# Performance work log

Hardware: AMD Instinct MI355X
Metric: run time of the kernel (lower is better)

## Reference

```python
import jax, jax.numpy as jnp
import numpy as np

B, N, M, F, D, OUT = 2, 8192, 8192, 128, 3, 512

def setup_inputs() -> dict:
    key = jax.random.key(0)
    k1, k2, k3, k4, k5 = jax.random.split(key, 5)
    return {
        'geometry': jax.random.normal(k1, (B, N, D), dtype=jnp.float32),
        'gaussian_pcd': jax.random.normal(k2, (B, M, D), dtype=jnp.float32),
        'features': jax.random.normal(k3, (B, M, F), dtype=jnp.float32),
        'W_proj': jax.random.normal(k4, (OUT, F), dtype=jnp.float32) / np.sqrt(F),
        'b_proj': jax.random.normal(k5, (OUT,), dtype=jnp.float32) * 0.01,
        'k': 10,
    }

def reference(geometry, gaussian_pcd, features, W_proj, b_proj, k):
    # cdist via ||q||^2 + ||p||^2 - 2 q.p (matches torch.cdist matmul mode)
    q2 = jnp.sum(geometry * geometry, axis=-1)            # [B,N]
    p2 = jnp.sum(gaussian_pcd * gaussian_pcd, axis=-1)    # [B,M]
    d2 = q2[:, :, None] + p2[:, None, :] - 2.0 * jnp.einsum('bnd,bmd->bnm', geometry, gaussian_pcd)
    dists = jnp.sqrt(jnp.maximum(d2, 0.0))                # [B,N,M]
    # k smallest, sorted ascending
    neg_d, idx = jax.lax.top_k(-dists, k)                 # [B,N,k]
    knn_d = -neg_d
    # gather knn features: [B,N,k,F]
    knn_f = jax.vmap(lambda f, i: f[i])(features, idx)
    # inverse-distance weights, normalized
    w = 1.0 / (knn_d + 1e-8)
    w = w / jnp.sum(w, axis=-1, keepdims=True)
    interp = jnp.einsum('bnk,bnkf->bnf', w, knn_f)        # [B,N,F]
    # gaussian_feature_proj: Linear(128 -> feature_dim)
    return jnp.einsum('bnf,of->bno', interp, W_proj) + b_proj
```

## Files before the change

### kernel.cpp

```cpp
#include <hip/hip_runtime.h>
#include <math.h>

#define NQ   8192
#define NP   8192
#define NF   128
#define NOUT 512
#define NB   2
#define KNN  10
#define BNQ  (NB*NQ)
#define QW   4

typedef unsigned long long u64;

__device__ __forceinline__ u64 shfl64(u64 v, int src) {
  unsigned lo = (unsigned)__shfl((int)(unsigned)(v & 0xffffffffull), src, 64);
  unsigned hi = (unsigned)__shfl((int)(unsigned)(v >> 32), src, 64);
  return ((u64)hi << 32) | lo;
}
__device__ __forceinline__ u64 shflup64(u64 v) {
  unsigned lo = (unsigned)__shfl_up((int)(unsigned)(v & 0xffffffffull), 1, 64);
  unsigned hi = (unsigned)__shfl_up((int)(unsigned)(v >> 32), 1, 64);
  return ((u64)hi << 32) | lo;
}

__device__ __forceinline__ float dist2m(float m2x, float m2y, float m2z,
                                        float q2c, float4 p) {
  return fmaf(m2x, p.x, fmaf(m2y, p.y, fmaf(m2z, p.z, q2c + p.w)));
}

__device__ __forceinline__ float wmin64f(float v) {
#pragma unroll
  for (int off = 1; off < 64; off <<= 1)
    v = fminf(v, __shfl_xor(v, off, 64));
  return v;
}

__global__ __launch_bounds__(256) void prep_kernel(
    const float* __restrict__ gpcd, const float* __restrict__ W,
    float4* __restrict__ pts4, float* __restrict__ Wt)
{
  int tid = blockIdx.x * 256 + threadIdx.x;
  if (tid < NB * NP) {
    const float* p = gpcd + (size_t)tid * 3;
    float x = p[0], y = p[1], z = p[2];
    float p2 = x * x + y * y + z * z;
    pts4[tid] = make_float4(x, y, z, p2);
  }
  int o = tid >> 7, f = tid & 127;
  Wt[(size_t)f * NOUT + o] = W[tid];
}

__global__ __launch_bounds__(256) void knn_interp_kernel(
    const float* __restrict__ geometry, const float4* __restrict__ pts4,
    const float* __restrict__ features, float* __restrict__ At)
{
  const int lane = threadIdx.x & 63;
  const int wave = (blockIdx.x << 2) | (threadIdx.x >> 6);
  const int q0   = wave * QW;
  const int b    = q0 >> 13;
  const float4* __restrict__ P = pts4 + ((size_t)b << 13);

  float m2x[QW], m2y[QW], m2z[QW], q2[QW];
#pragma unroll
  for (int j = 0; j < QW; ++j) {
    const float* g = geometry + (size_t)(q0 + j) * 3;
    float x = g[0], y = g[1], z = g[2];
    q2[j]  = x * x + y * y + z * z;
    m2x[j] = -2.0f * x; m2y[j] = -2.0f * y; m2z[j] = -2.0f * z;
  }

  float lmin[QW];
#pragma unroll
  for (int j = 0; j < QW; ++j) lmin[j] = INFINITY;
#pragma unroll 2
  for (int t = 0; t < NP / 64; ++t) {
    const float4 p = P[(t << 6) | lane];
#pragma unroll
    for (int j = 0; j < QW; ++j)
      lmin[j] = fminf(lmin[j], dist2m(m2x[j], m2y[j], m2z[j], q2[j], p));
  }
#pragma unroll
  for (int j = 0; j < QW; ++j) lmin[j] = fmaxf(lmin[j], 0.0f);

  float theta[QW];
#pragma unroll
  for (int j = 0; j < QW; ++j) {
    float lm  = lmin[j];
    float tau = 0.0f;
#pragma unroll
    for (int r = 0; r < KNN; ++r) {
      tau = wmin64f(lm);
      u64 mk = __ballot(lm == tau);
      int w  = __builtin_ctzll(mk);
      if (lane == w) lm = INFINITY;
    }
    theta[j] = __uint_as_float(__float_as_uint(tau) + 1);
  }

  u64   list[QW];
  float dl[QW];
#pragma unroll
  for (int j = 0; j < QW; ++j) {
    list[j] = 0x7F800000FFFFFFFFull;
    dl[j]   = INFINITY;
  }
  const float qnan = __builtin_nanf("");

  for (int t = 0; t < NP / 64; ++t) {
    const float4 p = P[(t << 6) | lane];
#pragma unroll
    for (int j = 0; j < QW; ++j) {
      float d2 = dist2m(m2x[j], m2y[j], m2z[j], q2[j], p);
      for (;;) {
        u64 mask = __ballot(d2 < theta[j]);
        if (!mask) break;
        int src = __builtin_ctzll(mask);
        float cd = __uint_as_float(
            (unsigned)__builtin_amdgcn_readlane(__float_as_int(d2), src));
        cd = fmaxf(cd, 0.0f);
        u64 kk = ((u64)__float_as_uint(cd) << 32) | (unsigned)((t << 6) + src);
        u64   prev  = shflup64(list[j]);
        float prevd = __shfl(dl[j], lane - 1, 64);
        bool mylt = list[j] < kk;
        bool pins = (lane == 0) || (prev < kk);
        list[j] = mylt ? list[j] : (pins ? kk : prev);
        dl[j]   = mylt ? dl[j]  : (pins ? cd : prevd);
        theta[j] = fminf(theta[j], __uint_as_float(
            (unsigned)__builtin_amdgcn_readlane(__float_as_int(dl[j]), 9)));
        if (lane == src) d2 = qnan;
      }
    }
  }

  const float* __restrict__ F = features + (size_t)b * NP * NF;
#pragma unroll
  for (int j = 0; j < QW; ++j) {
    float w = 1.0f / (sqrtf(dl[j]) + 1e-8f);
    float wsum = 0.0f;
#pragma unroll
    for (int jj = 0; jj < KNN; ++jj) wsum += __shfl(w, jj, 64);

    float a0 = 0.0f, a1 = 0.0f;
#pragma unroll
    for (int jj = 0; jj < KNN; ++jj) {
      float wj = __shfl(w, jj, 64) / wsum;
      int  mi  = (int)(unsigned)(shfl64(list[j], jj) & 0xffffffffull);
      const float2 f2 = *(const float2*)(F + (size_t)mi * NF + (lane << 1));
      a0 = fmaf(wj, f2.x, a0);
      a1 = fmaf(wj, f2.y, a1);
    }
    At[(size_t)(lane << 1) * BNQ + (q0 + j)]       = a0;
    At[(size_t)((lane << 1) + 1) * BNQ + (q0 + j)] = a1;
  }
}

#define PKC  64
#define PLD  68

__global__ __launch_bounds__(256) void proj_kernel(
    const float* __restrict__ At, const float* __restrict__ Wt,
    const float* __restrict__ bias, float* __restrict__ out)
{
  __shared__ __align__(16) float lds_a[PKC][PLD];
  __shared__ __align__(16) float lds_b[PKC][PLD];

  const int mt = blockIdx.x & 255;
  const int ot = blockIdx.x >> 8;
  const int tx = threadIdx.x & 15;
  const int ty = threadIdx.x >> 4;
  const int m0 = mt << 6;
  const int o0 = ot << 6;

  const int lr = threadIdx.x >> 4;
  const int lc = (threadIdx.x & 15) << 2;

  float acc[4][4];
#pragma unroll
  for (int i = 0; i < 4; ++i)
#pragma unroll
    for (int jj = 0; jj < 4; ++jj) acc[i][jj] = 0.0f;

#pragma unroll
  for (int kc = 0; kc < NF / PKC; ++kc) {
    const int k0 = kc * PKC;
#pragma unroll
    for (int rp = 0; rp < 4; ++rp) {
      const int r = (rp << 4) + lr;
      const float4 a4 = *(const float4*)(At + (size_t)(k0 + r) * BNQ  + m0 + lc);
      const float4 b4 = *(const float4*)(Wt + (size_t)(k0 + r) * NOUT + o0 + lc);
      *(float4*)(&lds_a[r][lc]) = a4;
      *(float4*)(&lds_b[r][lc]) = b4;
    }
    __syncthreads();
#pragma unroll 8
    for (int k = 0; k < PKC; ++k) {
      const float4 a  = *(const float4*)(&lds_a[k][ty << 2]);
      const float4 bv = *(const float4*)(&lds_b[k][tx << 2]);
      float av[4] = {a.x, a.y, a.z, a.w};
      float bw[4] = {bv.x, bv.y, bv.z, bv.w};
#pragma unroll
      for (int i = 0; i < 4; ++i)
#pragma unroll
        for (int jj = 0; jj < 4; ++jj)
          acc[i][jj] = fmaf(av[i], bw[jj], acc[i][jj]);
    }
    __syncthreads();
  }

  const float4 bb = *(const float4*)(bias + o0 + (tx << 2));
  float bias4[4] = {bb.x, bb.y, bb.z, bb.w};
#pragma unroll
  for (int i = 0; i < 4; ++i) {
    float4 r;
    r.x = acc[i][0] + bias4[0];
    r.y = acc[i][1] + bias4[1];
    r.z = acc[i][2] + bias4[2];
    r.w = acc[i][3] + bias4[3];
    *(float4*)(out + (size_t)(m0 + (ty << 2) + i) * NOUT + o0 + (tx << 2)) = r;
  }
}

extern "C" void kernel_launch(void* const* d_in, const int* in_sizes, int n_in,
                              void* d_out, int out_size, void* d_ws, size_t ws_size,
                              hipStream_t stream) {
  const float* geometry = (const float*)d_in[0];
  const float* gpcd     = (const float*)d_in[1];
  const float* features = (const float*)d_in[2];
  const float* W        = (const float*)d_in[3];
  const float* bias     = (const float*)d_in[4];
  float* out = (float*)d_out;

  char*   ws   = (char*)d_ws;
  float*  At   = (float*)ws;
  float4* pts4 = (float4*)(ws + (size_t)NF * BNQ * 4);
  float*  Wt   = (float*)(ws + (size_t)NF * BNQ * 4 + (size_t)NB * NP * 16);

  prep_kernel<<<256, 256, 0, stream>>>(gpcd, W, pts4, Wt);
  knn_interp_kernel<<<BNQ / (QW * 4), 256, 0, stream>>>(geometry, pts4, features, At);
  proj_kernel<<<(BNQ / 64) * (NOUT / 64), 256, 0, stream>>>(At, Wt, bias, out);
}
```

Baseline: 130.3 us.

## Split point scan across two waves per query group and merge top-k lists

Each group of four queries is now processed by two waves, each scanning half of the point cloud and building its own sorted top-k list. The two partial lists are written to shared memory and merged with a rank-based merge, then each wave performs the feature gather for two of the four queries. This doubles the number of waves to improve latency hiding and occupancy on the long distance scan. In exchange it adds block synchronization and a merge step, and the per-half threshold is looser so more insertion iterations may occur.

```diff
diff --git a/kernel.cpp b/kernel.cpp
--- a/kernel.cpp
+++ b/kernel.cpp
@@ -3,6 +3,7 @@
 
 #define NQ   8192
 #define NP   8192
+#define NPH  4096
 #define NF   128
 #define NOUT 512
 #define NB   2
@@ -12,11 +13,6 @@
 
 typedef unsigned long long u64;
 
-__device__ __forceinline__ u64 shfl64(u64 v, int src) {
-  unsigned lo = (unsigned)__shfl((int)(unsigned)(v & 0xffffffffull), src, 64);
-  unsigned hi = (unsigned)__shfl((int)(unsigned)(v >> 32), src, 64);
-  return ((u64)hi << 32) | lo;
-}
 __device__ __forceinline__ u64 shflup64(u64 v) {
   unsigned lo = (unsigned)__shfl_up((int)(unsigned)(v & 0xffffffffull), 1, 64);
   unsigned hi = (unsigned)__shfl_up((int)(unsigned)(v >> 32), 1, 64);
@@ -33,6 +29,28 @@
   for (int off = 1; off < 64; off <<= 1)
     v = fminf(v, __shfl_xor(v, off, 64));
   return v;
+}
+
+__device__ __forceinline__ void insert_loop(float d2, int idxbase, int lane,
+                                            u64& lst, float& dlv, float& th) {
+  for (;;) {
+    u64 mask = __ballot(d2 < th);
+    if (!mask) break;
+    int src = __builtin_ctzll(mask);
+    float cd = __uint_as_float(
+        (unsigned)__builtin_amdgcn_readlane(__float_as_int(d2), src));
+    cd = fmaxf(cd, 0.0f);
+    u64 kk = ((u64)__float_as_uint(cd) << 32) | (unsigned)(idxbase + src);
+    u64   prev  = shflup64(lst);
+    float prevd = __shfl(dlv, lane - 1, 64);
+    bool mylt = lst < kk;
+    bool pins = (lane == 0) || (prev < kk);
+    lst = mylt ? lst : (pins ? kk : prev);
+    dlv = mylt ? dlv : (pins ? cd : prevd);
+    th = fminf(th, __uint_as_float(
+        (unsigned)__builtin_amdgcn_readlane(__float_as_int(dlv), 9)));
+    if (lane == src) d2 = __builtin_nanf("");
+  }
 }
 
 __global__ __launch_bounds__(256) void prep_kernel(
@@ -54,17 +72,23 @@
     const float* __restrict__ geometry, const float4* __restrict__ pts4,
     const float* __restrict__ features, float* __restrict__ At)
 {
+  __shared__ u64 cand[2][QW][2][12];
+  __shared__ u64 merged[2][2][2][12];
+
   const int lane = threadIdx.x & 63;
-  const int wave = (blockIdx.x << 2) | (threadIdx.x >> 6);
-  const int q0   = wave * QW;
+  const int wid  = threadIdx.x >> 6;
+  const int g    = wid >> 1;
+  const int h    = wid & 1;
+  const int q0   = (blockIdx.x * 2 + g) * QW;
   const int b    = q0 >> 13;
-  const float4* __restrict__ P = pts4 + ((size_t)b << 13);
+  const float4* __restrict__ Ph = pts4 + ((size_t)b << 13) + (h << 12);
+  const int hbase = h << 12;
 
   float m2x[QW], m2y[QW], m2z[QW], q2[QW];
 #pragma unroll
   for (int j = 0; j < QW; ++j) {
-    const float* g = geometry + (size_t)(q0 + j) * 3;
-    float x = g[0], y = g[1], z = g[2];
+    const float* gp = geometry + (size_t)(q0 + j) * 3;
+    float x = gp[0], y = gp[1], z = gp[2];
     q2[j]  = x * x + y * y + z * z;
     m2x[j] = -2.0f * x; m2y[j] = -2.0f * y; m2z[j] = -2.0f * z;
   }
@@ -72,12 +96,14 @@
   float lmin[QW];
 #pragma unroll
   for (int j = 0; j < QW; ++j) lmin[j] = INFINITY;
-#pragma unroll 2
-  for (int t = 0; t < NP / 64; ++t) {
-    const float4 p = P[(t << 6) | lane];
+  for (int t = 0; t < NPH / 128; ++t) {
+    const float4 pa = Ph[(t << 7) | lane];
+    const float4 pb = Ph[(t << 7) | 64 | lane];
 #pragma unroll
     for (int j = 0; j < QW; ++j)
-      lmin[j] = fminf(lmin[j], dist2m(m2x[j], m2y[j], m2z[j], q2[j], p));
+      lmin[j] = fminf(lmin[j],
+                      fminf(dist2m(m2x[j], m2y[j], m2z[j], q2[j], pa),
+                            dist2m(m2x[j], m2y[j], m2z[j], q2[j], pb)));
   }
 #pragma unroll
   for (int j = 0; j < QW; ++j) lmin[j] = fmaxf(lmin[j], 0.0f);
@@ -104,53 +130,67 @@
     list[j] = 0x7F800000FFFFFFFFull;
     dl[j]   = INFINITY;
   }
-  const float qnan = __builtin_nanf("");
-
-  for (int t = 0; t < NP / 64; ++t) {
-    const float4 p = P[(t << 6) | lane];
+
+  for (int t = 0; t < NPH / 128; ++t) {
+    const float4 pa = Ph[(t << 7) | lane];
+    const float4 pb = Ph[(t << 7) | 64 | lane];
 #pragma unroll
     for (int j = 0; j < QW; ++j) {
-      float d2 = dist2m(m2x[j], m2y[j], m2z[j], q2[j], p);
-      for (;;) {
-        u64 mask = __ballot(d2 < theta[j]);
-        if (!mask) break;
-        int src = __builtin_ctzll(mask);
-        float cd = __uint_as_float(
-            (unsigned)__builtin_amdgcn_readlane(__float_as_int(d2), src));
-        cd = fmaxf(cd, 0.0f);
-        u64 kk = ((u64)__float_as_uint(cd) << 32) | (unsigned)((t << 6) + src);
-        u64   prev  = shflup64(list[j]);
-        float prevd = __shfl(dl[j], lane - 1, 64);
-        bool mylt = list[j] < kk;
-        bool pins = (lane == 0) || (prev < kk);
-        list[j] = mylt ? list[j] : (pins ? kk : prev);
-        dl[j]   = mylt ? dl[j]  : (pins ? cd : prevd);
-        theta[j] = fminf(theta[j], __uint_as_float(
-            (unsigned)__builtin_amdgcn_readlane(__float_as_int(dl[j]), 9)));
-        if (lane == src) d2 = qnan;
+      float da = dist2m(m2x[j], m2y[j], m2z[j], q2[j], pa);
+      insert_loop(da, hbase + (t << 7), lane, list[j], dl[j], theta[j]);
+      float db = dist2m(m2x[j], m2y[j], m2z[j], q2[j], pb);
+      insert_loop(db, hbase + (t << 7) + 64, lane, list[j], dl[j], theta[j]);
+    }
+  }
+
+#pragma unroll
+  for (int j = 0; j < QW; ++j)
+    if (lane < KNN) cand[g][j][h][lane] = list[j];
+  __syncthreads();
+
+#pragma unroll
+  for (int jo = 0; jo < 2; ++jo) {
+    const int jj = (h << 1) | jo;
+    const bool isA = lane < KNN;
+    const bool isB = (lane >= 16) && (lane < 16 + KNN);
+    const int  li  = isA ? lane : lane - 16;
+    if (isA | isB) {
+      u64 key = cand[g][jj][isA ? 0 : 1][li];
+      int pos = li;
+#pragma unroll
+      for (int m = 0; m < KNN; ++m) {
+        u64 other = cand[g][jj][isA ? 1 : 0][m];
+        pos += (other < key) ? 1 : 0;
       }
-    }
-  }
+      if (pos < KNN) merged[g][h][jo][pos] = key;
+    }
+  }
+  __syncthreads();
 
   const float* __restrict__ F = features + (size_t)b * NP * NF;
 #pragma unroll
-  for (int j = 0; j < QW; ++j) {
-    float w = 1.0f / (sqrtf(dl[j]) + 1e-8f);
+  for (int jo = 0; jo < 2; ++jo) {
+    u64 k = merged[g][h][jo][lane < KNN ? lane : 0];
+    float mdl = __uint_as_float((unsigned)(k >> 32));
+    int  midx = (int)(unsigned)(k & 0xffffffffull);
+
+    float w = 1.0f / (sqrtf(mdl) + 1e-8f);
     float wsum = 0.0f;
 #pragma unroll
-    for (int jj = 0; jj < KNN; ++jj) wsum += __shfl(w, jj, 64);
+    for (int jj2 = 0; jj2 < KNN; ++jj2) wsum += __shfl(w, jj2, 64);
 
     float a0 = 0.0f, a1 = 0.0f;
 #pragma unroll
-    for (int jj = 0; jj < KNN; ++jj) {
-      float wj = __shfl(w, jj, 64) / wsum;
-      int  mi  = (int)(unsigned)(shfl64(list[j], jj) & 0xffffffffull);
+    for (int jj2 = 0; jj2 < KNN; ++jj2) {
+      float wj = __shfl(w, jj2, 64) / wsum;
+      int  mi  = __shfl(midx, jj2, 64);
       const float2 f2 = *(const float2*)(F + (size_t)mi * NF + (lane << 1));
       a0 = fmaf(wj, f2.x, a0);
       a1 = fmaf(wj, f2.y, a1);
     }
-    At[(size_t)(lane << 1) * BNQ + (q0 + j)]       = a0;
-    At[(size_t)((lane << 1) + 1) * BNQ + (q0 + j)] = a1;
+    const int q = q0 + (h << 1) + jo;
+    At[(size_t)(lane << 1) * BNQ + q]       = a0;
+    At[(size_t)((lane << 1) + 1) * BNQ + q] = a1;
   }
 }
 
@@ -236,6 +276,6 @@
   float*  Wt   = (float*)(ws + (size_t)NF * BNQ * 4 + (size_t)NB * NP * 16);
 
   prep_kernel<<<256, 256, 0, stream>>>(gpcd, W, pts4, Wt);
-  knn_interp_kernel<<<BNQ / (QW * 4), 256, 0, stream>>>(geometry, pts4, features, At);
+  knn_interp_kernel<<<BNQ / 8, 256, 0, stream>>>(geometry, pts4, features, At);
   proj_kernel<<<(BNQ / 64) * (NOUT / 64), 256, 0, stream>>>(At, Wt, bias, out);
 }
```

Result: slower. 151.2 us (+16.0%).

## Drop per-query norm from distance scan and add wave-level early-skip check

Applied to the files above, without the earlier changes.

Distances are computed without the query's squared norm, which is constant per query and does not change the ordering. Signed values are handled by a monotone float-to-uint key, and the norm is added back only when the final weights are computed. The point scan now loads four points per iteration. A cheap ballot over the minimum across the four queries skips the per-query insertion loops when no lane can beat any threshold. This cuts FMAs and ballot overhead in the second pass, at the cost of more registers and more intricate handling of negative-threshold edge cases.

```diff
diff --git a/kernel.cpp b/kernel.cpp
--- a/kernel.cpp
+++ b/kernel.cpp
@@ -23,9 +23,14 @@
   return ((u64)hi << 32) | lo;
 }
 
-__device__ __forceinline__ float dist2m(float m2x, float m2y, float m2z,
-                                        float q2c, float4 p) {
-  return fmaf(m2x, p.x, fmaf(m2y, p.y, fmaf(m2z, p.z, q2c + p.w)));
+__device__ __forceinline__ float dist2s(float m2x, float m2y, float m2z,
+                                        float4 p) {
+  return fmaf(m2x, p.x, fmaf(m2y, p.y, fmaf(m2z, p.z, p.w)));
+}
+
+__device__ __forceinline__ unsigned fmono(float f) {
+  unsigned u = __float_as_uint(f);
+  return u ^ ((unsigned)((int)u >> 31) | 0x80000000u);
 }
 
 __device__ __forceinline__ float wmin64f(float v) {
@@ -33,6 +38,27 @@
   for (int off = 1; off < 64; off <<= 1)
     v = fminf(v, __shfl_xor(v, off, 64));
   return v;
+}
+
+__device__ __forceinline__ void insert_loop(float d2, int idxbase, int lane,
+                                            u64& lst, float& dlv, float& th) {
+  for (;;) {
+    u64 mask = __ballot(d2 < th);
+    if (!mask) break;
+    int src = __builtin_ctzll(mask);
+    float cd = __uint_as_float(
+        (unsigned)__builtin_amdgcn_readlane(__float_as_int(d2), src));
+    u64 kk = ((u64)fmono(cd) << 32) | (unsigned)(idxbase + src);
+    u64   prev  = shflup64(lst);
+    float prevd = __shfl(dlv, lane - 1, 64);
+    bool mylt = lst < kk;
+    bool pins = (lane == 0) || (prev < kk);
+    lst = mylt ? lst : (pins ? kk : prev);
+    dlv = mylt ? dlv : (pins ? cd : prevd);
+    th = fminf(th, __uint_as_float(
+        (unsigned)__builtin_amdgcn_readlane(__float_as_int(dlv), 9)));
+    if (lane == src) d2 = __builtin_nanf("");
+  }
 }
 
 __global__ __launch_bounds__(256) void prep_kernel(
@@ -58,7 +84,7 @@
   const int wave = (blockIdx.x << 2) | (threadIdx.x >> 6);
   const int q0   = wave * QW;
   const int b    = q0 >> 13;
-  const float4* __restrict__ P = pts4 + ((size_t)b << 13);
+  const float4* __restrict__ P = pts4 + ((size_t)b << 13) + lane;
 
   float m2x[QW], m2y[QW], m2z[QW], q2[QW];
 #pragma unroll
@@ -72,15 +98,19 @@
   float lmin[QW];
 #pragma unroll
   for (int j = 0; j < QW; ++j) lmin[j] = INFINITY;
-#pragma unroll 2
-  for (int t = 0; t < NP / 64; ++t) {
-    const float4 p = P[(t << 6) | lane];
-#pragma unroll
-    for (int j = 0; j < QW; ++j)
-      lmin[j] = fminf(lmin[j], dist2m(m2x[j], m2y[j], m2z[j], q2[j], p));
-  }
-#pragma unroll
-  for (int j = 0; j < QW; ++j) lmin[j] = fmaxf(lmin[j], 0.0f);
+  for (int t = 0; t < NP / 256; ++t) {
+    float4 pv[4];
+#pragma unroll
+    for (int s = 0; s < 4; ++s) pv[s] = P[(t << 8) + (s << 6)];
+#pragma unroll
+    for (int j = 0; j < QW; ++j) {
+      float d0 = dist2s(m2x[j], m2y[j], m2z[j], pv[0]);
+      float d1 = dist2s(m2x[j], m2y[j], m2z[j], pv[1]);
+      float d2 = dist2s(m2x[j], m2y[j], m2z[j], pv[2]);
+      float d3 = dist2s(m2x[j], m2y[j], m2z[j], pv[3]);
+      lmin[j] = fminf(lmin[j], fminf(fminf(d0, d1), fminf(d2, d3)));
+    }
+  }
 
   float theta[QW];
 #pragma unroll
@@ -94,40 +124,37 @@
       int w  = __builtin_ctzll(mk);
       if (lane == w) lm = INFINITY;
     }
-    theta[j] = __uint_as_float(__float_as_uint(tau) + 1);
-  }
+    unsigned tb = __float_as_uint(tau);
+    unsigned nb = (tb & 0x80000000u) ? (tb == 0x80000000u ? 1u : tb - 1u)
+                                     : tb + 1u;
+    theta[j] = __uint_as_float(nb);
+  }
+  float thmax = fmaxf(fmaxf(theta[0], theta[1]), fmaxf(theta[2], theta[3]));
 
   u64   list[QW];
   float dl[QW];
 #pragma unroll
   for (int j = 0; j < QW; ++j) {
-    list[j] = 0x7F800000FFFFFFFFull;
+    list[j] = 0xFF800000FFFFFFFFull;
     dl[j]   = INFINITY;
   }
-  const float qnan = __builtin_nanf("");
-
-  for (int t = 0; t < NP / 64; ++t) {
-    const float4 p = P[(t << 6) | lane];
-#pragma unroll
-    for (int j = 0; j < QW; ++j) {
-      float d2 = dist2m(m2x[j], m2y[j], m2z[j], q2[j], p);
-      for (;;) {
-        u64 mask = __ballot(d2 < theta[j]);
-        if (!mask) break;
-        int src = __builtin_ctzll(mask);
-        float cd = __uint_as_float(
-            (unsigned)__builtin_amdgcn_readlane(__float_as_int(d2), src));
-        cd = fmaxf(cd, 0.0f);
-        u64 kk = ((u64)__float_as_uint(cd) << 32) | (unsigned)((t << 6) + src);
-        u64   prev  = shflup64(list[j]);
-        float prevd = __shfl(dl[j], lane - 1, 64);
-        bool mylt = list[j] < kk;
-        bool pins = (lane == 0) || (prev < kk);
-        list[j] = mylt ? list[j] : (pins ? kk : prev);
-        dl[j]   = mylt ? dl[j]  : (pins ? cd : prevd);
-        theta[j] = fminf(theta[j], __uint_as_float(
-            (unsigned)__builtin_amdgcn_readlane(__float_as_int(dl[j]), 9)));
-        if (lane == src) d2 = qnan;
+
+  for (int t = 0; t < NP / 256; ++t) {
+    float4 pv[4];
+#pragma unroll
+    for (int s = 0; s < 4; ++s) pv[s] = P[(t << 8) + (s << 6)];
+#pragma unroll
+    for (int s = 0; s < 4; ++s) {
+      float d[QW];
+#pragma unroll
+      for (int j = 0; j < QW; ++j)
+        d[j] = dist2s(m2x[j], m2y[j], m2z[j], pv[s]);
+      float pmin = fminf(fminf(d[0], d[1]), fminf(d[2], d[3]));
+      if (__ballot(pmin < thmax)) {
+#pragma unroll
+        for (int j = 0; j < QW; ++j)
+          insert_loop(d[j], (t << 8) + (s << 6), lane, list[j], dl[j], theta[j]);
+        thmax = fmaxf(fmaxf(theta[0], theta[1]), fmaxf(theta[2], theta[3]));
       }
     }
   }
@@ -135,7 +162,8 @@
   const float* __restrict__ F = features + (size_t)b * NP * NF;
 #pragma unroll
   for (int j = 0; j < QW; ++j) {
-    float w = 1.0f / (sqrtf(dl[j]) + 1e-8f);
+    float td2 = fmaxf(dl[j] + q2[j], 0.0f);
+    float w   = 1.0f / (sqrtf(td2) + 1e-8f);
     float wsum = 0.0f;
 #pragma unroll
     for (int jj = 0; jj < KNN; ++jj) wsum += __shfl(w, jj, 64);
```

Result: slower. 144.6 us (+11.0%).

## Replace FP32 SIMT projection with bf16 MFMA GEMM and bf16 intermediate

Applied to the files above, without the earlier changes.

The interpolated features and projection weights are now stored as bf16 in row-major layout, and the output projection uses 16x16x32 bf16 MFMA instructions that read operands directly from global memory instead of an LDS-tiled FP32 FMA loop. This is meant to cut the projection GEMM's compute time and halve the intermediate buffer's traffic. In exchange it lowers precision to bf16 for the GEMM inputs, and the output stores are scattered per element rather than vectorised. The KNN search stage, which likely dominates total time, is unchanged.

```diff
diff --git a/kernel.cpp b/kernel.cpp
--- a/kernel.cpp
+++ b/kernel.cpp
@@ -11,6 +11,9 @@
 #define QW   4
 
 typedef unsigned long long u64;
+typedef unsigned short ushort_t;
+typedef __attribute__((ext_vector_type(8))) short bf16x8;
+typedef __attribute__((ext_vector_type(4))) float f32x4;
 
 __device__ __forceinline__ u64 shfl64(u64 v, int src) {
   unsigned lo = (unsigned)__shfl((int)(unsigned)(v & 0xffffffffull), src, 64);
@@ -35,9 +38,14 @@
   return v;
 }
 
+__device__ __forceinline__ ushort_t f2bf(float x) {
+  unsigned u = __float_as_uint(x);
+  return (ushort_t)((u + 0x7FFFu + ((u >> 16) & 1u)) >> 16);
+}
+
 __global__ __launch_bounds__(256) void prep_kernel(
     const float* __restrict__ gpcd, const float* __restrict__ W,
-    float4* __restrict__ pts4, float* __restrict__ Wt)
+    float4* __restrict__ pts4, ushort_t* __restrict__ Wb)
 {
   int tid = blockIdx.x * 256 + threadIdx.x;
   if (tid < NB * NP) {
@@ -46,13 +54,12 @@
     float p2 = x * x + y * y + z * z;
     pts4[tid] = make_float4(x, y, z, p2);
   }
-  int o = tid >> 7, f = tid & 127;
-  Wt[(size_t)f * NOUT + o] = W[tid];
+  Wb[tid] = f2bf(W[tid]);
 }
 
 __global__ __launch_bounds__(256) void knn_interp_kernel(
     const float* __restrict__ geometry, const float4* __restrict__ pts4,
-    const float* __restrict__ features, float* __restrict__ At)
+    const float* __restrict__ features, ushort_t* __restrict__ Abf)
 {
   const int lane = threadIdx.x & 63;
   const int wave = (blockIdx.x << 2) | (threadIdx.x >> 6);
@@ -149,74 +156,61 @@
       a0 = fmaf(wj, f2.x, a0);
       a1 = fmaf(wj, f2.y, a1);
     }
-    At[(size_t)(lane << 1) * BNQ + (q0 + j)]       = a0;
-    At[(size_t)((lane << 1) + 1) * BNQ + (q0 + j)] = a1;
-  }
-}
-
-#define PKC  64
-#define PLD  68
-
-__global__ __launch_bounds__(256) void proj_kernel(
-    const float* __restrict__ At, const float* __restrict__ Wt,
+    unsigned pack = (unsigned)f2bf(a0) | ((unsigned)f2bf(a1) << 16);
+    *(unsigned*)(Abf + (size_t)(q0 + j) * NF + (lane << 1)) = pack;
+  }
+}
+
+__global__ __launch_bounds__(256) void proj_mfma(
+    const ushort_t* __restrict__ Abf, const ushort_t* __restrict__ Wb,
     const float* __restrict__ bias, float* __restrict__ out)
 {
-  __shared__ __align__(16) float lds_a[PKC][PLD];
-  __shared__ __align__(16) float lds_b[PKC][PLD];
-
-  const int mt = blockIdx.x & 255;
-  const int ot = blockIdx.x >> 8;
-  const int tx = threadIdx.x & 15;
-  const int ty = threadIdx.x >> 4;
-  const int m0 = mt << 6;
-  const int o0 = ot << 6;
-
-  const int lr = threadIdx.x >> 4;
-  const int lc = (threadIdx.x & 15) << 2;
-
-  float acc[4][4];
+  const int lane = threadIdx.x & 63;
+  const int w    = threadIdx.x >> 6;
+  const int mt   = blockIdx.x & 127;
+  const int ot   = blockIdx.x >> 7;
+  const int m0   = (mt << 7) + ((w & 1) << 6);
+  const int o0   = (ot << 6) + ((w >> 1) << 5);
+  const int r    = lane & 15;
+  const int kg   = (lane >> 4) << 3;
+
+  f32x4 acc[4][2];
 #pragma unroll
   for (int i = 0; i < 4; ++i)
 #pragma unroll
-    for (int jj = 0; jj < 4; ++jj) acc[i][jj] = 0.0f;
-
-#pragma unroll
-  for (int kc = 0; kc < NF / PKC; ++kc) {
-    const int k0 = kc * PKC;
-#pragma unroll
-    for (int rp = 0; rp < 4; ++rp) {
-      const int r = (rp << 4) + lr;
-      const float4 a4 = *(const float4*)(At + (size_t)(k0 + r) * BNQ  + m0 + lc);
-      const float4 b4 = *(const float4*)(Wt + (size_t)(k0 + r) * NOUT + o0 + lc);
-      *(float4*)(&lds_a[r][lc]) = a4;
-      *(float4*)(&lds_b[r][lc]) = b4;
-    }
-    __syncthreads();
-#pragma unroll 8
-    for (int k = 0; k < PKC; ++k) {
-      const float4 a  = *(const float4*)(&lds_a[k][ty << 2]);
-      const float4 bv = *(const float4*)(&lds_b[k][tx << 2]);
-      float av[4] = {a.x, a.y, a.z, a.w};
-      float bw[4] = {bv.x, bv.y, bv.z, bv.w};
-#pragma unroll
-      for (int i = 0; i < 4; ++i)
-#pragma unroll
-        for (int jj = 0; jj < 4; ++jj)
-          acc[i][jj] = fmaf(av[i], bw[jj], acc[i][jj]);
-    }
-    __syncthreads();
-  }
-
-  const float4 bb = *(const float4*)(bias + o0 + (tx << 2));
-  float bias4[4] = {bb.x, bb.y, bb.z, bb.w};
-#pragma unroll
-  for (int i = 0; i < 4; ++i) {
-    float4 r;
-    r.x = acc[i][0] + bias4[0];
-    r.y = acc[i][1] + bias4[1];
-    r.z = acc[i][2] + bias4[2];
-    r.w = acc[i][3] + bias4[3];
-    *(float4*)(out + (size_t)(m0 + (ty << 2) + i) * NOUT + o0 + (tx << 2)) = r;
+    for (int jn = 0; jn < 2; ++jn) acc[i][jn] = (f32x4)0.0f;
+
+#pragma unroll
+  for (int ks = 0; ks < 4; ++ks) {
+    const int k0 = (ks << 5) + kg;
+    bf16x8 a[4], bb[2];
+#pragma unroll
+    for (int i = 0; i < 4; ++i)
+      a[i] = *(const bf16x8*)(Abf + (size_t)(m0 + (i << 4) + r) * NF + k0);
+#pragma unroll
+    for (int jn = 0; jn < 2; ++jn)
+      bb[jn] = *(const bf16x8*)(Wb + (size_t)(o0 + (jn << 4) + r) * NF + k0);
+#pragma unroll
+    for (int i = 0; i < 4; ++i)
+#pragma unroll
+      for (int jn = 0; jn < 2; ++jn)
+        acc[i][jn] = __builtin_amdgcn_mfma_f32_16x16x32_bf16(
+            a[i], bb[jn], acc[i][jn], 0, 0, 0);
+  }
+
+  const int crow = (lane >> 4) << 2;
+#pragma unroll
+  for (int jn = 0; jn < 2; ++jn) {
+    const int oc = o0 + (jn << 4) + r;
+    const float bv = bias[oc];
+#pragma unroll
+    for (int i = 0; i < 4; ++i) {
+#pragma unroll
+      for (int reg = 0; reg < 4; ++reg) {
+        const int qm = m0 + (i << 4) + crow + reg;
+        out[(size_t)qm * NOUT + oc] = acc[i][jn][reg] + bv;
+      }
+    }
   }
 }
 
@@ -230,12 +224,12 @@
   const float* bias     = (const float*)d_in[4];
   float* out = (float*)d_out;
 
-  char*   ws   = (char*)d_ws;
-  float*  At   = (float*)ws;
-  float4* pts4 = (float4*)(ws + (size_t)NF * BNQ * 4);
-  float*  Wt   = (float*)(ws + (size_t)NF * BNQ * 4 + (size_t)NB * NP * 16);
-
-  prep_kernel<<<256, 256, 0, stream>>>(gpcd, W, pts4, Wt);
-  knn_interp_kernel<<<BNQ / (QW * 4), 256, 0, stream>>>(geometry, pts4, features, At);
-  proj_kernel<<<(BNQ / 64) * (NOUT / 64), 256, 0, stream>>>(At, Wt, bias, out);
-}
+  char*     ws   = (char*)d_ws;
+  ushort_t* Abf  = (ushort_t*)ws;
+  float4*   pts4 = (float4*)(ws + (size_t)BNQ * NF * 2);
+  ushort_t* Wb   = (ushort_t*)(ws + (size_t)BNQ * NF * 2 + (size_t)NB * NP * 16);
+
+  prep_kernel<<<256, 256, 0, stream>>>(gpcd, W, pts4, Wb);
+  knn_interp_kernel<<<BNQ / (QW * 4), 256, 0, stream>>>(geometry, pts4, features, Abf);
+  proj_mfma<<<(BNQ / 128) * (NOUT / 64), 256, 0, stream>>>(Abf, Wb, bias, out);
+}
```

Result: faster. 114.0 us (-12.6%).
